# Kernel optimization log

Measured on AMD Instinct MI355X. Metric: run time of the kernel, lower is better.

The kernel has to match this reference:

```python
import jax, jax.numpy as jnp
import numpy as np

N, D = 4096, 128  # seq length / feature dim of x is N; head dim is D

def setup_inputs() -> dict:
    key = jax.random.key(0)
    k1, k2 = jax.random.split(key)
    x = jax.random.normal(k1, (N, N), dtype=jnp.float32)
    # nn.Linear(N, 3*d): weight [3d, N], bias [3d]; scale weight like torch init
    W = jax.random.normal(k2, (3 * D, N), dtype=jnp.float32) / jnp.sqrt(jnp.float32(N))
    b = jnp.zeros((3 * D,), dtype=jnp.float32)
    return {"x": x, "W": W, "b": b}

def reference(x, W, b):
    # QKV projection: [N, 3d]
    qkv = x @ W.T + b
    Q, K, V = jnp.split(qkv, 3, axis=-1)  # each [N, d]
    # The blockwise online-softmax double loop computes exactly
    # softmax(Q K^T) V with NO 1/sqrt(d) scaling (faithful to source).
    S = Q @ K.T                 # [N, N]
    P = jax.nn.softmax(S, axis=-1)
    return P @ V                # [N, d]
```

## Files before the change

### kernel.cpp

```cpp
#include <hip/hip_runtime.h>
#include <cstdint>
#include <cstddef>

typedef _Float16 f16;
typedef f16 f16x8 __attribute__((ext_vector_type(8)));
typedef f16 f16x4 __attribute__((ext_vector_type(4)));
typedef float f32x4 __attribute__((ext_vector_type(4)));

#define SEQ 4096
#define DH 128
#define QKV_LD 384
#define LOG2E 1.44269504f
#define DEFER_THR 4.0f

__device__ __forceinline__ float fast_exp2(float x) {
#if __has_builtin(__builtin_amdgcn_exp2f)
  return __builtin_amdgcn_exp2f(x);
#else
  return exp2f(x);
#endif
}

__device__ __forceinline__ void gl_lds16(const void* g, void* l) {
  __builtin_amdgcn_global_load_lds((const __attribute__((address_space(1))) void*)g,
                                   (__attribute__((address_space(3))) void*)l, 16, 0, 0);
}

__global__ __launch_bounds__(256) void cvt_w_kernel(const float4* __restrict__ W,
                                                    f16x4* __restrict__ Wh) {
  int i = blockIdx.x * 256 + threadIdx.x;
  float4 v = W[i];
  f16x4 h; h[0] = (f16)v.x; h[1] = (f16)v.y; h[2] = (f16)v.z; h[3] = (f16)v.w;
  Wh[i] = h;
}

template <int SPLITS>
__global__ __launch_bounds__(256, 2) void gemm_qkv(const float* __restrict__ x,
                                                   const f16* __restrict__ Wh,
                                                   f16* __restrict__ part) {
  __shared__ __align__(16) f16 Ax[64][136];
  __shared__ __align__(16) f16 Bx[QKV_LD * 64];
  const int m0 = blockIdx.x * 64;
  const int split = blockIdx.y;
  const int kc = SEQ / SPLITS;
  const int k0 = split * kc;
  const int tid = threadIdx.x;
  const int lane = tid & 63;
  const int wave = tid >> 6;
  const int nb = wave * 96;
  const int l15 = lane & 15, quad = lane >> 4;

  f32x4 acc[4][6] = {};
  float4 areg[8];

#define LOAD_A(KT)                                                         \
  do {                                                                     \
    _Pragma("unroll") for (int r = 0; r < 8; ++r) {                        \
      int c = r * 256 + tid;                                               \
      int row = c >> 5, col = (c & 31) * 4;                                \
      areg[r] = *(const float4*)&x[(size_t)(m0 + row) * SEQ + (KT) + col]; \
    }                                                                      \
  } while (0)

  LOAD_A(k0);

  for (int kt = k0; kt < k0 + kc; kt += 128) {
#pragma unroll
    for (int r = 0; r < 8; ++r) {
      int c = r * 256 + tid;
      int row = c >> 5, col = (c & 31) * 4;
      f16x4 h; h[0] = (f16)areg[r].x; h[1] = (f16)areg[r].y;
      h[2] = (f16)areg[r].z; h[3] = (f16)areg[r].w;
      *(f16x4*)&Ax[row][col] = h;
    }
    const bool nextA = (kt + 128 < k0 + kc);
#pragma unroll
    for (int h = 0; h < 2; ++h) {
#pragma unroll
      for (int r = 0; r < 12; ++r) {
        int c = r * 256 + tid;
        int row = c >> 3, ch = c & 7;
        const f16* src = &Wh[(size_t)row * SEQ + kt + h * 64 + ((ch ^ (row & 7)) << 3)];
        gl_lds16(src, &Bx[(size_t)c << 3]);
      }
      __syncthreads();
      if (h == 0 && nextA) LOAD_A(kt + 128);
#pragma unroll
      for (int ks = 0; ks < 2; ++ks) {
        f16x8 a[4], bb[6];
#pragma unroll
        for (int t = 0; t < 4; ++t)
          a[t] = *(const f16x8*)&Ax[t * 16 + l15][h * 64 + ks * 32 + quad * 8];
#pragma unroll
        for (int t = 0; t < 6; ++t) {
          int n = nb + t * 16 + l15;
          int ch = (ks * 4 + quad) ^ (l15 & 7);
          bb[t] = *(const f16x8*)&Bx[((size_t)n << 6) + (ch << 3)];
        }
#pragma unroll
        for (int mt = 0; mt < 4; ++mt)
#pragma unroll
          for (int nt = 0; nt < 6; ++nt)
            acc[mt][nt] = __builtin_amdgcn_mfma_f32_16x16x32_f16(a[mt], bb[nt], acc[mt][nt], 0, 0, 0);
      }
      __syncthreads();
    }
  }
#undef LOAD_A

  f16* pw = part + (((size_t)split * 64 + blockIdx.x) * 24) * 256 * 4;
#pragma unroll
  for (int mt = 0; mt < 4; ++mt) {
#pragma unroll
    for (int nt = 0; nt < 6; ++nt) {
      int p = mt * 6 + nt;
      f16x4 h;
#pragma unroll
      for (int rr = 0; rr < 4; ++rr) h[rr] = (f16)acc[mt][nt][rr];
      *(f16x4*)&pw[((size_t)p * 256 + tid) * 4] = h;
    }
  }
}

template <int SPLITS>
__global__ __launch_bounds__(256) void reduce_qkv(const f16* __restrict__ part,
                                                  const float* __restrict__ bias,
                                                  f16* __restrict__ qkv,
                                                  f16* __restrict__ Vt) {
  __shared__ __align__(16) f16 Vl[128][24];
  const int bx = blockIdx.x;
  const int mt = blockIdx.y;
  const int tid = threadIdx.x;
  const int lane = tid & 63, wave = tid >> 6;
  const int l15 = lane & 15, quad = lane >> 4;
  const int rowl = quad * 4;
  const int rowbase = bx * 64 + mt * 16 + rowl;

#pragma unroll
  for (int nt = 0; nt < 6; ++nt) {
    const int p = mt * 6 + nt;
    float acc[4] = {0.f, 0.f, 0.f, 0.f};
#pragma unroll
    for (int s = 0; s < SPLITS; ++s) {
      f16x4 v = *(const f16x4*)&part[((((size_t)s * 64 + bx) * 24 + p) * 256 + tid) * 4];
#pragma unroll
      for (int rr = 0; rr < 4; ++rr) acc[rr] += (float)v[rr];
    }
    int col = wave * 96 + nt * 16 + l15;
    float bv = bias[col];
    if (col < 128) {
#pragma unroll
      for (int rr = 0; rr < 4; ++rr)
        qkv[(size_t)(rowbase + rr) * QKV_LD + col] = (f16)((acc[rr] + bv) * LOG2E);
    } else if (col < 256) {
#pragma unroll
      for (int rr = 0; rr < 4; ++rr)
        qkv[(size_t)(rowbase + rr) * QKV_LD + col] = (f16)(acc[rr] + bv);
    } else {
      f16x4 h;
#pragma unroll
      for (int rr = 0; rr < 4; ++rr) h[rr] = (f16)(acc[rr] + bv);
      *(f16x4*)&Vl[col - 256][rowl] = h;
    }
  }
  __syncthreads();
  {
    int d = tid >> 1, seg = tid & 1;
    f16x8 v = *(const f16x8*)&Vl[d][seg * 8];
    *(f16x8*)&Vt[(size_t)d * SEQ + bx * 64 + mt * 16 + seg * 8] = v;
  }
}

#define NSPLIT 16
#define KVRANGE (SEQ / NSPLIT)

__global__ __launch_bounds__(256, 2) void attn_partial(const f16* __restrict__ qkv,
                                                       const f16* __restrict__ Vt,
                                                       f16* __restrict__ Op,
                                                       float* __restrict__ ml) {
  __shared__ __align__(16) f16 smem[27136];
  f16* Ks = smem;
  f16* Vs = smem + 8704;
  f16* Ps = smem + 17920;

  const int q0 = blockIdx.x * 128;
  const int split = blockIdx.y;
  const int kv0 = split * KVRANGE;
  const int tid = threadIdx.x;
  const int lane = tid & 63, wave = tid >> 6;
  const int l15 = lane & 15, quad = lane >> 4;
  const int mbase = q0 + wave * 32;
  f16* Psw = Ps + wave * 32 * 72;

  f16x8 qf[2][4];
#pragma unroll
  for (int mt = 0; mt < 2; ++mt)
#pragma unroll
    for (int ks = 0; ks < 4; ++ks)
      qf[mt][ks] = *(const f16x8*)&qkv[(size_t)(mbase + mt * 16 + l15) * QKV_LD + ks * 32 + quad * 8];

  f32x4 oacc[2][8] = {};
  float mrow[2] = {-1e30f, -1e30f};
  float lrow[2] = {0.f, 0.f};

  f16x8 kreg[4], vreg[4];
#define LOAD_TILE(K0)                                                                  \
  do {                                                                                 \
    _Pragma("unroll") for (int r = 0; r < 4; ++r) {                                    \
      int c = tid + r * 256;                                                           \
      int row = c >> 4, col = (c & 15) * 8;                                            \
      kreg[r] = *(const f16x8*)&qkv[(size_t)((K0) + row) * QKV_LD + DH + col];         \
    }                                                                                  \
    _Pragma("unroll") for (int r = 0; r < 4; ++r) {                                    \
      int c = tid + r * 256;                                                           \
      int row = c >> 3, col = (c & 7) * 8;                                             \
      vreg[r] = *(const f16x8*)&Vt[(size_t)row * SEQ + (K0) + col];                    \
    }                                                                                  \
  } while (0)

  LOAD_TILE(kv0);

  for (int it = 0; it < KVRANGE / 64; ++it) {
#pragma unroll
    for (int r = 0; r < 4; ++r) {
      int c = tid + r * 256;
      int row = c >> 4, col = (c & 15) * 8;
      *(f16x8*)&Ks[row * 136 + col] = kreg[r];
    }
#pragma unroll
    for (int r = 0; r < 4; ++r) {
      int c = tid + r * 256;
      int row = c >> 3, col = (c & 7) * 8;
      *(f16x8*)&Vs[row * 72 + col] = vreg[r];
    }
    __syncthreads();
    if (it + 1 < KVRANGE / 64) { int k0n = kv0 + (it + 1) * 64; LOAD_TILE(k0n); }

    f32x4 st[4][2] = {};
    __builtin_amdgcn_s_setprio(1);
#pragma unroll
    for (int ks = 0; ks < 4; ++ks) {
      f16x8 kf[4];
#pragma unroll
      for (int kt = 0; kt < 4; ++kt)
        kf[kt] = *(const f16x8*)&Ks[(kt * 16 + l15) * 136 + ks * 32 + quad * 8];
#pragma unroll
      for (int kt = 0; kt < 4; ++kt)
#pragma unroll
        for (int mt = 0; mt < 2; ++mt)
          st[kt][mt] = __builtin_amdgcn_mfma_f32_16x16x32_f16(kf[kt], qf[mt][ks], st[kt][mt], 0, 0, 0);
    }
    __builtin_amdgcn_s_setprio(0);

    float vmax[2];
#pragma unroll
    for (int mt = 0; mt < 2; ++mt) {
      float v = -1e30f;
#pragma unroll
      for (int kt = 0; kt < 4; ++kt)
#pragma unroll
        for (int rr = 0; rr < 4; ++rr) v = fmaxf(v, st[kt][mt][rr]);
      v = fmaxf(v, __shfl_xor(v, 16));
      v = fmaxf(v, __shfl_xor(v, 32));
      vmax[mt] = v;
    }
    bool ok = (vmax[0] <= mrow[0] + DEFER_THR) & (vmax[1] <= mrow[1] + DEFER_THR);
    if (!__all(ok)) {
      float al[2];
#pragma unroll
      for (int mt = 0; mt < 2; ++mt) {
        float mnew = fmaxf(mrow[mt], vmax[mt]);
        al[mt] = fast_exp2(mrow[mt] - mnew);
        mrow[mt] = mnew;
        lrow[mt] *= al[mt];
      }
      float alr[2][4];
#pragma unroll
      for (int mt = 0; mt < 2; ++mt)
#pragma unroll
        for (int rr = 0; rr < 4; ++rr)
          alr[mt][rr] = __shfl(al[mt], quad * 4 + rr);
#pragma unroll
      for (int mt = 0; mt < 2; ++mt)
#pragma unroll
        for (int dt = 0; dt < 8; ++dt)
#pragma unroll
          for (int rr = 0; rr < 4; ++rr)
            oacc[mt][dt][rr] *= alr[mt][rr];
    }
#pragma unroll
    for (int mt = 0; mt < 2; ++mt) {
      float ls = 0.f;
#pragma unroll
      for (int kt = 0; kt < 4; ++kt) {
        f16x4 pk;
#pragma unroll
        for (int rr = 0; rr < 4; ++rr) {
          float p = fast_exp2(st[kt][mt][rr] - mrow[mt]);
          ls += p;
          pk[rr] = (f16)p;
        }
        *(f16x4*)&Psw[(mt * 16 + l15) * 72 + kt * 16 + quad * 4] = pk;
      }
      ls += __shfl_xor(ls, 16);
      ls += __shfl_xor(ls, 32);
      lrow[mt] += ls;
    }

    __builtin_amdgcn_s_setprio(1);
#pragma unroll
    for (int kk = 0; kk < 2; ++kk) {
      f16x8 pf[2];
#pragma unroll
      for (int mt = 0; mt < 2; ++mt)
        pf[mt] = *(const f16x8*)&Psw[(mt * 16 + l15) * 72 + kk * 32 + quad * 8];
#pragma unroll
      for (int dt = 0; dt < 8; ++dt) {
        f16x8 vf = *(const f16x8*)&Vs[(dt * 16 + l15) * 72 + kk * 32 + quad * 8];
#pragma unroll
        for (int mt = 0; mt < 2; ++mt)
          oacc[mt][dt] = __builtin_amdgcn_mfma_f32_16x16x32_f16(pf[mt], vf, oacc[mt][dt], 0, 0, 0);
      }
    }
    __builtin_amdgcn_s_setprio(0);
    __syncthreads();
  }
#undef LOAD_TILE

  f16* Os = smem;
#pragma unroll
  for (int mt = 0; mt < 2; ++mt)
#pragma unroll
    for (int dt = 0; dt < 8; ++dt)
#pragma unroll
      for (int rr = 0; rr < 4; ++rr)
        Os[(wave * 32 + mt * 16 + quad * 4 + rr) * 136 + dt * 16 + l15] = (f16)oacc[mt][dt][rr];
  if (quad == 0) {
#pragma unroll
    for (int mt = 0; mt < 2; ++mt) {
      int row = mbase + mt * 16 + l15;
      ml[((size_t)split * SEQ + row) * 2 + 0] = mrow[mt];
      ml[((size_t)split * SEQ + row) * 2 + 1] = lrow[mt];
    }
  }
  __syncthreads();
#pragma unroll
  for (int j = 0; j < 8; ++j) {
    int c = j * 256 + tid;
    int row = c >> 4, ch = c & 15;
    f16x8 v = *(const f16x8*)&Os[row * 136 + ch * 8];
    *(f16x8*)&Op[((size_t)split * SEQ + q0 + row) * DH + ch * 8] = v;
  }
}

__global__ __launch_bounds__(256) void combine_kernel(const f16* __restrict__ Op,
                                                      const float* __restrict__ ml,
                                                      float* __restrict__ out) {
  int t = blockIdx.x * 256 + threadIdx.x;
  int base = t * 8;
  int row = base >> 7;
  float ms[NSPLIT], ls[NSPLIT];
  float M = -1e30f;
#pragma unroll
  for (int s = 0; s < NSPLIT; ++s) {
    float2 v = *(const float2*)&ml[((size_t)s * SEQ + row) * 2];
    ms[s] = v.x; ls[s] = v.y;
    M = fmaxf(M, v.x);
  }
  float L = 0.f;
  float o[8] = {};
#pragma unroll
  for (int s = 0; s < NSPLIT; ++s) {
    float w = fast_exp2(ms[s] - M);
    L += ls[s] * w;
    f16x8 v = *(const f16x8*)&Op[(size_t)s * SEQ * DH + base];
#pragma unroll
    for (int j = 0; j < 8; ++j) o[j] += w * (float)v[j];
  }
  float inv = 1.0f / L;
  float4 o0, o1;
  o0.x = o[0] * inv; o0.y = o[1] * inv; o0.z = o[2] * inv; o0.w = o[3] * inv;
  o1.x = o[4] * inv; o1.y = o[5] * inv; o1.z = o[6] * inv; o1.w = o[7] * inv;
  *(float4*)&out[base] = o0;
  *(float4*)&out[base + 4] = o1;
}

extern "C" void kernel_launch(void* const* d_in, const int* in_sizes, int n_in,
                              void* d_out, int out_size, void* d_ws, size_t ws_size,
                              hipStream_t stream) {
  const float* x = (const float*)d_in[0];
  const float* W = (const float*)d_in[1];
  const float* b = (const float*)d_in[2];
  float* out = (float*)d_out;
  char* ws = (char*)d_ws;

  f16*   Wh   = (f16*)(ws);
  f16*   qkv  = (f16*)(ws + (3u << 20));
  f16*   Vt   = (f16*)(ws + (6u << 20));
  float* ml   = (float*)(ws + (7u << 20));
  char*  scr  = ws + (7u << 20) + (1u << 19);
  f16*   part = (f16*)scr;
  f16*   Op   = (f16*)scr;

  cvt_w_kernel<<<(384 * 4096 / 4) / 256, 256, 0, stream>>>((const float4*)W, (f16x4*)Wh);

  bool big = ws_size >= ((size_t)31u << 20) + ((size_t)1u << 19);
  if (big) {
    gemm_qkv<8><<<dim3(SEQ / 64, 8), 256, 0, stream>>>(x, Wh, part);
    reduce_qkv<8><<<dim3(64, 4), 256, 0, stream>>>(part, b, qkv, Vt);
  } else {
    gemm_qkv<4><<<dim3(SEQ / 64, 4), 256, 0, stream>>>(x, Wh, part);
    reduce_qkv<4><<<dim3(64, 4), 256, 0, stream>>>(part, b, qkv, Vt);
  }
  attn_partial<<<dim3(SEQ / 128, NSPLIT), 256, 0, stream>>>(qkv, Vt, Op, ml);
  combine_kernel<<<(SEQ * DH) / 8 / 256, 256, 0, stream>>>(Op, ml, out);
}
```

Measured before the change: 143.5 us.

## Fuse split-K reduction into QKV GEMM via last-block atomic counter

```diff
diff --git a/kernel.cpp b/kernel.cpp
--- a/kernel.cpp
+++ b/kernel.cpp
@@ -27,20 +27,31 @@
 }
 
 __global__ __launch_bounds__(256) void cvt_w_kernel(const float4* __restrict__ W,
-                                                    f16x4* __restrict__ Wh) {
+                                                    f16x4* __restrict__ Wh,
+                                                    int* __restrict__ cnt) {
   int i = blockIdx.x * 256 + threadIdx.x;
+  if (blockIdx.x == 0 && threadIdx.x < 64) cnt[threadIdx.x] = 0;
   float4 v = W[i];
   f16x4 h; h[0] = (f16)v.x; h[1] = (f16)v.y; h[2] = (f16)v.z; h[3] = (f16)v.w;
   Wh[i] = h;
 }
 
 template <int SPLITS>
-__global__ __launch_bounds__(256, 2) void gemm_qkv(const float* __restrict__ x,
-                                                   const f16* __restrict__ Wh,
-                                                   f16* __restrict__ part) {
-  __shared__ __align__(16) f16 Ax[64][136];
-  __shared__ __align__(16) f16 Bx[QKV_LD * 64];
-  const int m0 = blockIdx.x * 64;
+__global__ __launch_bounds__(256, 2) void gemm_qkv_fused(const float* __restrict__ x,
+                                                         const f16* __restrict__ Wh,
+                                                         const float* __restrict__ bias,
+                                                         f16* __restrict__ part,
+                                                         int* __restrict__ cnt,
+                                                         f16* __restrict__ qkv,
+                                                         f16* __restrict__ Vt) {
+  __shared__ __align__(16) char smem_raw[66560];
+  f16 (*Ax)[136] = (f16(*)[136])smem_raw;
+  f16* Bx = (f16*)(smem_raw + 17408);
+  f16 (*Vl)[72] = (f16(*)[72])(smem_raw + 17408);
+  __shared__ int amLast;
+
+  const int bx = blockIdx.x;
+  const int m0 = bx * 64;
   const int split = blockIdx.y;
   const int kc = SEQ / SPLITS;
   const int k0 = split * kc;
@@ -108,7 +119,7 @@
   }
 #undef LOAD_A
 
-  f16* pw = part + (((size_t)split * 64 + blockIdx.x) * 24) * 256 * 4;
+  f16* pw = part + (((size_t)split * 64 + bx) * 24) * 256 * 4;
 #pragma unroll
   for (int mt = 0; mt < 4; ++mt) {
 #pragma unroll
@@ -120,54 +131,55 @@
       *(f16x4*)&pw[((size_t)p * 256 + tid) * 4] = h;
     }
   }
-}
-
-template <int SPLITS>
-__global__ __launch_bounds__(256) void reduce_qkv(const f16* __restrict__ part,
-                                                  const float* __restrict__ bias,
-                                                  f16* __restrict__ qkv,
-                                                  f16* __restrict__ Vt) {
-  __shared__ __align__(16) f16 Vl[128][24];
-  const int bx = blockIdx.x;
-  const int mt = blockIdx.y;
-  const int tid = threadIdx.x;
-  const int lane = tid & 63, wave = tid >> 6;
-  const int l15 = lane & 15, quad = lane >> 4;
-  const int rowl = quad * 4;
-  const int rowbase = bx * 64 + mt * 16 + rowl;
-
-#pragma unroll
-  for (int nt = 0; nt < 6; ++nt) {
-    const int p = mt * 6 + nt;
-    float acc[4] = {0.f, 0.f, 0.f, 0.f};
-#pragma unroll
-    for (int s = 0; s < SPLITS; ++s) {
-      f16x4 v = *(const f16x4*)&part[((((size_t)s * 64 + bx) * 24 + p) * 256 + tid) * 4];
-#pragma unroll
-      for (int rr = 0; rr < 4; ++rr) acc[rr] += (float)v[rr];
-    }
-    int col = wave * 96 + nt * 16 + l15;
-    float bv = bias[col];
-    if (col < 128) {
-#pragma unroll
-      for (int rr = 0; rr < 4; ++rr)
-        qkv[(size_t)(rowbase + rr) * QKV_LD + col] = (f16)((acc[rr] + bv) * LOG2E);
-    } else if (col < 256) {
-#pragma unroll
-      for (int rr = 0; rr < 4; ++rr)
-        qkv[(size_t)(rowbase + rr) * QKV_LD + col] = (f16)(acc[rr] + bv);
-    } else {
-      f16x4 h;
-#pragma unroll
-      for (int rr = 0; rr < 4; ++rr) h[rr] = (f16)(acc[rr] + bv);
-      *(f16x4*)&Vl[col - 256][rowl] = h;
-    }
+
+  __threadfence();
+  if (tid == 0) {
+    int c = atomicAdd(&cnt[bx], 1);
+    amLast = (c == SPLITS - 1);
   }
   __syncthreads();
-  {
-    int d = tid >> 1, seg = tid & 1;
+  if (!amLast) return;
+  __threadfence();
+
+#pragma unroll
+  for (int mt = 0; mt < 4; ++mt) {
+    const int rowl = mt * 16 + quad * 4;
+    const int rowbase = m0 + rowl;
+#pragma unroll
+    for (int nt = 0; nt < 6; ++nt) {
+      const int p = mt * 6 + nt;
+      float racc[4] = {0.f, 0.f, 0.f, 0.f};
+#pragma unroll
+      for (int s = 0; s < SPLITS; ++s) {
+        f16x4 v = *(const f16x4*)&part[((((size_t)s * 64 + bx) * 24 + p) * 256 + tid) * 4];
+#pragma unroll
+        for (int rr = 0; rr < 4; ++rr) racc[rr] += (float)v[rr];
+      }
+      int col = nb + nt * 16 + l15;
+      float bv = bias[col];
+      if (col < 128) {
+#pragma unroll
+        for (int rr = 0; rr < 4; ++rr)
+          qkv[(size_t)(rowbase + rr) * QKV_LD + col] = (f16)((racc[rr] + bv) * LOG2E);
+      } else if (col < 256) {
+#pragma unroll
+        for (int rr = 0; rr < 4; ++rr)
+          qkv[(size_t)(rowbase + rr) * QKV_LD + col] = (f16)(racc[rr] + bv);
+      } else {
+        f16x4 h;
+#pragma unroll
+        for (int rr = 0; rr < 4; ++rr) h[rr] = (f16)(racc[rr] + bv);
+        *(f16x4*)&Vl[col - 256][rowl] = h;
+      }
+    }
+  }
+  __syncthreads();
+#pragma unroll
+  for (int j = 0; j < 4; ++j) {
+    int c = j * 256 + tid;
+    int d = c >> 3, seg = c & 7;
     f16x8 v = *(const f16x8*)&Vl[d][seg * 8];
-    *(f16x8*)&Vt[(size_t)d * SEQ + bx * 64 + mt * 16 + seg * 8] = v;
+    *(f16x8*)&Vt[(size_t)d * SEQ + m0 + seg * 8] = v;
   }
 }
 
@@ -399,18 +411,17 @@
   f16*   Vt   = (f16*)(ws + (6u << 20));
   float* ml   = (float*)(ws + (7u << 20));
   char*  scr  = ws + (7u << 20) + (1u << 19);
-  f16*   part = (f16*)scr;
-  f16*   Op   = (f16*)scr;
-
-  cvt_w_kernel<<<(384 * 4096 / 4) / 256, 256, 0, stream>>>((const float4*)W, (f16x4*)Wh);
-
-  bool big = ws_size >= ((size_t)31u << 20) + ((size_t)1u << 19);
+  int*   cnt  = (int*)scr;
+  f16*   part = (f16*)(scr + 4096);
+  f16*   Op   = (f16*)(scr + 4096);
+
+  cvt_w_kernel<<<(384 * 4096 / 4) / 256, 256, 0, stream>>>((const float4*)W, (f16x4*)Wh, cnt);
+
+  bool big = ws_size >= ((size_t)31u << 20) + ((size_t)1u << 19) + 4096;
   if (big) {
-    gemm_qkv<8><<<dim3(SEQ / 64, 8), 256, 0, stream>>>(x, Wh, part);
-    reduce_qkv<8><<<dim3(64, 4), 256, 0, stream>>>(part, b, qkv, Vt);
+    gemm_qkv_fused<8><<<dim3(SEQ / 64, 8), 256, 0, stream>>>(x, Wh, b, part, cnt, qkv, Vt);
   } else {
-    gemm_qkv<4><<<dim3(SEQ / 64, 4), 256, 0, stream>>>(x, Wh, part);
-    reduce_qkv<4><<<dim3(64, 4), 256, 0, stream>>>(part, b, qkv, Vt);
+    gemm_qkv_fused<4><<<dim3(SEQ / 64, 4), 256, 0, stream>>>(x, Wh, b, part, cnt, qkv, Vt);
   }
   attn_partial<<<dim3(SEQ / 128, NSPLIT), 256, 0, stream>>>(qkv, Vt, Op, ml);
   combine_kernel<<<(SEQ * DH) / 8 / 256, 256, 0, stream>>>(Op, ml, out);
```

Measured after the change: 224.1 us. 56.2% more time.

## Read K and V fragments directly from global memory instead of staging in LDS

Applied to the files above, without the earlier changes.

```diff
diff --git a/kernel.cpp b/kernel.cpp
--- a/kernel.cpp
+++ b/kernel.cpp
@@ -178,10 +178,7 @@
                                                        const f16* __restrict__ Vt,
                                                        f16* __restrict__ Op,
                                                        float* __restrict__ ml) {
-  __shared__ __align__(16) f16 smem[27136];
-  f16* Ks = smem;
-  f16* Vs = smem + 8704;
-  f16* Ps = smem + 17920;
+  __shared__ __align__(16) f16 smem[17408];
 
   const int q0 = blockIdx.x * 128;
   const int split = blockIdx.y;
@@ -190,7 +187,7 @@
   const int lane = tid & 63, wave = tid >> 6;
   const int l15 = lane & 15, quad = lane >> 4;
   const int mbase = q0 + wave * 32;
-  f16* Psw = Ps + wave * 32 * 72;
+  f16* Psw = smem + wave * 32 * 72;
 
   f16x8 qf[2][4];
 #pragma unroll
@@ -203,38 +200,8 @@
   float mrow[2] = {-1e30f, -1e30f};
   float lrow[2] = {0.f, 0.f};
 
-  f16x8 kreg[4], vreg[4];
-#define LOAD_TILE(K0)                                                                  \
-  do {                                                                                 \
-    _Pragma("unroll") for (int r = 0; r < 4; ++r) {                                    \
-      int c = tid + r * 256;                                                           \
-      int row = c >> 4, col = (c & 15) * 8;                                            \
-      kreg[r] = *(const f16x8*)&qkv[(size_t)((K0) + row) * QKV_LD + DH + col];         \
-    }                                                                                  \
-    _Pragma("unroll") for (int r = 0; r < 4; ++r) {                                    \
-      int c = tid + r * 256;                                                           \
-      int row = c >> 3, col = (c & 7) * 8;                                             \
-      vreg[r] = *(const f16x8*)&Vt[(size_t)row * SEQ + (K0) + col];                    \
-    }                                                                                  \
-  } while (0)
-
-  LOAD_TILE(kv0);
-
   for (int it = 0; it < KVRANGE / 64; ++it) {
-#pragma unroll
-    for (int r = 0; r < 4; ++r) {
-      int c = tid + r * 256;
-      int row = c >> 4, col = (c & 15) * 8;
-      *(f16x8*)&Ks[row * 136 + col] = kreg[r];
-    }
-#pragma unroll
-    for (int r = 0; r < 4; ++r) {
-      int c = tid + r * 256;
-      int row = c >> 3, col = (c & 7) * 8;
-      *(f16x8*)&Vs[row * 72 + col] = vreg[r];
-    }
-    __syncthreads();
-    if (it + 1 < KVRANGE / 64) { int k0n = kv0 + (it + 1) * 64; LOAD_TILE(k0n); }
+    const int k0 = kv0 + it * 64;
 
     f32x4 st[4][2] = {};
     __builtin_amdgcn_s_setprio(1);
@@ -243,7 +210,7 @@
       f16x8 kf[4];
 #pragma unroll
       for (int kt = 0; kt < 4; ++kt)
-        kf[kt] = *(const f16x8*)&Ks[(kt * 16 + l15) * 136 + ks * 32 + quad * 8];
+        kf[kt] = *(const f16x8*)&qkv[(size_t)(k0 + kt * 16 + l15) * QKV_LD + DH + ks * 32 + quad * 8];
 #pragma unroll
       for (int kt = 0; kt < 4; ++kt)
 #pragma unroll
@@ -316,25 +283,15 @@
         pf[mt] = *(const f16x8*)&Psw[(mt * 16 + l15) * 72 + kk * 32 + quad * 8];
 #pragma unroll
       for (int dt = 0; dt < 8; ++dt) {
-        f16x8 vf = *(const f16x8*)&Vs[(dt * 16 + l15) * 72 + kk * 32 + quad * 8];
+        f16x8 vf = *(const f16x8*)&Vt[(size_t)(dt * 16 + l15) * SEQ + k0 + kk * 32 + quad * 8];
 #pragma unroll
         for (int mt = 0; mt < 2; ++mt)
           oacc[mt][dt] = __builtin_amdgcn_mfma_f32_16x16x32_f16(pf[mt], vf, oacc[mt][dt], 0, 0, 0);
       }
     }
     __builtin_amdgcn_s_setprio(0);
-    __syncthreads();
-  }
-#undef LOAD_TILE
-
-  f16* Os = smem;
-#pragma unroll
-  for (int mt = 0; mt < 2; ++mt)
-#pragma unroll
-    for (int dt = 0; dt < 8; ++dt)
-#pragma unroll
-      for (int rr = 0; rr < 4; ++rr)
-        Os[(wave * 32 + mt * 16 + quad * 4 + rr) * 136 + dt * 16 + l15] = (f16)oacc[mt][dt][rr];
+  }
+
   if (quad == 0) {
 #pragma unroll
     for (int mt = 0; mt < 2; ++mt) {
@@ -343,6 +300,15 @@
       ml[((size_t)split * SEQ + row) * 2 + 1] = lrow[mt];
     }
   }
+  __syncthreads();
+  f16* Os = smem;
+#pragma unroll
+  for (int mt = 0; mt < 2; ++mt)
+#pragma unroll
+    for (int dt = 0; dt < 8; ++dt)
+#pragma unroll
+      for (int rr = 0; rr < 4; ++rr)
+        Os[(wave * 32 + mt * 16 + quad * 4 + rr) * 136 + dt * 16 + l15] = (f16)oacc[mt][dt][rr];
   __syncthreads();
 #pragma unroll
   for (int j = 0; j < 8; ++j) {
```

New measurement: 164.8 us. 14.9% more time.
